# Performance work log

Hardware: AMD Instinct MI355X
Metric: run time of the kernel (lower is better)

Reference implementation:

```python
import jax, jax.numpy as jnp
import numpy as np

# Module hyperparameters (from init_kwargs)
B, C, T, H, W = 2, 128, 4, 64, 64
NHEADS = 32
SH, SW = 4, 4          # scales: patch size in H and W
GROUPS = C // 4        # GroupNorm groups = dim // 4
EPS = 1e-5


def _rel_index(t_, h_, w_):
    """(N,N) int32 index into the (2T-1)*(2h-1)*(2w-1) relative-position table."""
    tt = np.arange(t_); yy = np.arange(h_); xx = np.arange(w_)
    coords = np.stack(np.meshgrid(tt, yy, xx, indexing='ij'), -1).reshape(-1, 3)  # (N,3)
    rel = coords[:, None, :] - coords[None, :, :]                                 # (N,N,3)
    rel = rel + np.array([t_ - 1, h_ - 1, w_ - 1])
    idx = (rel[..., 0] * (2 * h_ - 1) + rel[..., 1]) * (2 * w_ - 1) + rel[..., 2]
    return idx.astype(np.int32)


def setup_inputs() -> dict:
    key = jax.random.key(0)
    ks = jax.random.split(key, 6)
    h, w = H // SH, W // SW
    table_sz = (2 * T - 1) * (2 * h - 1) * (2 * w - 1)
    inp = {
        "x": jax.random.normal(ks[0], (B, C, T, H, W), jnp.float32),
        "Wq": jax.random.normal(ks[1], (C, C), jnp.float32) / np.sqrt(C).astype(np.float32),
        "Wk": jax.random.normal(ks[2], (C, C), jnp.float32) / np.sqrt(C).astype(np.float32),
        "Wv": jax.random.normal(ks[3], (C, C), jnp.float32) / np.sqrt(C).astype(np.float32),
        "gq_gamma": jnp.ones((C,), jnp.float32), "gq_beta": jnp.zeros((C,), jnp.float32),
        "gk_gamma": jnp.ones((C,), jnp.float32), "gk_beta": jnp.zeros((C,), jnp.float32),
        "gv_gamma": jnp.ones((C,), jnp.float32), "gv_beta": jnp.zeros((C,), jnp.float32),
        "rel_table": jax.random.normal(ks[4], (NHEADS, table_sz), jnp.float32) * 0.02,
        "rel_index": jnp.asarray(_rel_index(T, h, w)),
    }
    return inp


def _group_norm(z, gamma, beta, groups, eps=EPS):
    b, c = z.shape[:2]
    zg = z.reshape(b, groups, c // groups, *z.shape[2:])
    mu = zg.mean(axis=(2, 3, 4, 5), keepdims=True)
    var = jnp.mean(jnp.square(zg - mu), axis=(2, 3, 4, 5), keepdims=True)
    zg = (zg - mu) * jax.lax.rsqrt(var + eps)
    zn = zg.reshape(z.shape)
    return zn * gamma[None, :, None, None, None] + beta[None, :, None, None, None]


def reference(x, Wq, Wk, Wv, gq_gamma, gq_beta, gk_gamma, gk_beta,
              gv_gamma, gv_beta, rel_table, rel_index):
    b, c, t, hh, ww = x.shape
    h, w = hh // SH, ww // SW
    n = t * h * w           # patch tokens
    p = SH * SW             # pixels per patch
    d = c // NHEADS         # head dim

    # 1x1x1 projections (pointwise conv == channel matmul) + GroupNorm
    q = _group_norm(jnp.einsum('bcthw,oc->bothw', x, Wq), gq_gamma, gq_beta, GROUPS)
    k = _group_norm(jnp.einsum('bcthw,oc->bothw', x, Wk), gk_gamma, gk_beta, GROUPS)
    v = _group_norm(jnp.einsum('bcthw,oc->bothw', x, Wv), gv_gamma, gv_beta, GROUPS)

    def to_patches(z):  # (b,c,t,H,W) -> (b,heads,d,N,P)
        z = z.reshape(b, NHEADS, d, t, h, SH, w, SW)
        z = z.transpose(0, 1, 2, 3, 4, 6, 5, 7)
        return z.reshape(b, NHEADS, d, n, p)

    qp = to_patches(q).mean(-1)     # pooled patch queries (b,g,d,N)
    kp = to_patches(k).mean(-1)     # pooled patch keys    (b,g,d,N)
    vp = to_patches(v)              # full-res values      (b,g,d,N,P)

    scale = 1.0 / jnp.sqrt(jnp.float32(d))
    logits = jnp.einsum('bgdn,bgdm->bgnm', qp, kp) * scale
    logits = logits + rel_table[:, rel_index][None]   # relative position bias (1,g,N,N)
    attn = jax.nn.softmax(logits, axis=-1)

    out = jnp.einsum('bgnm,bgdmp->bgdnp', attn, vp)   # (b,g,d,N,P)
    out = out.reshape(b, NHEADS, d, t, h, w, SH, SW).transpose(0, 1, 2, 3, 4, 6, 5, 7)
    out = out.reshape(b, c, t, hh, ww)                # (B,C,T,H,W) after outer permute
    return out
```

## Files before the change

kernel.cpp:

```cpp
#include <hip/hip_runtime.h>
#include <hip/hip_bf16.h>

#define B_ 2
#define C_ 128
#define G_ 32
#define N_ 1024
#define S_ 16384
#define TABLE_ 6727
#define EPS_ 1e-5f
#define LOG2E_ 1.44269504f
#define PSTB_ 64

typedef __hip_bfloat16 bf16;
typedef __attribute__((ext_vector_type(8))) short short8;
typedef __attribute__((ext_vector_type(4))) float f32x4;

#if __has_builtin(__builtin_amdgcn_exp2f)
#define EXP2(x) __builtin_amdgcn_exp2f(x)
#else
#define EXP2(x) __expf((x) * 0.69314718056f)
#endif

__device__ __forceinline__ float bf2f(bf16 v) { return __bfloat162float(v); }
__device__ __forceinline__ float bits2f(unsigned u) { return __uint_as_float(u); }
__device__ __forceinline__ int dflag(const void* gq) {
  return (((const unsigned*)gq)[0] != 0x3F803F80u) ? 1 : 0;
}
__device__ __forceinline__ float ldcv(const void* p, int i, int fl) {
  return fl ? ((const float*)p)[i] : bf2f(((const bf16*)p)[i]);
}

__global__ __launch_bounds__(256) void proj_kernel(
    const void* __restrict__ x, const void* __restrict__ Wq,
    const void* __restrict__ Wk, const void* __restrict__ Wv,
    const void* __restrict__ gq,
    bf16* __restrict__ qraw, bf16* __restrict__ kraw, bf16* __restrict__ vpt,
    float* __restrict__ statsAcc)
{
  __shared__ bf16 xs[128 * 128];
  __shared__ bf16 vs[8192];
  const int tid = threadIdx.x, lane = tid & 63, w = tid >> 6;
  const int s0 = blockIdx.x * 128;
  const int oh = blockIdx.y;
  const int b  = blockIdx.z;
  const int fl = dflag(gq);

  {
    const int s_lo = tid & 15, cb = tid >> 4;
    const size_t gc = (size_t)b * C_ * S_ + (size_t)(cb * 8) * S_ + s0 + s_lo;
#pragma unroll
    for (int i = 0; i < 8; ++i) {
      const int s = i * 16 + s_lo;
      union { short8 v; bf16 h[8]; } u;
      if (fl) {
#pragma unroll
        for (int j = 0; j < 8; ++j)
          u.h[j] = (bf16)((const float*)x)[gc + i * 16 + (size_t)j * S_];
      } else {
#pragma unroll
        for (int j = 0; j < 8; ++j)
          u.h[j] = ((const bf16*)x)[gc + i * 16 + (size_t)j * S_];
      }
      *(short8*)&xs[s * 128 + ((cb ^ (s & 7)) << 3)] = u.v;
    }
  }

  const int ow = oh * 4 + w;
  const int quad = lane >> 4;
  const int om = ow * 16 + (lane & 15);
  const void* const Ws[3] = {Wq, Wk, Wv};
  short8 afr[3][4];
#pragma unroll
  for (int tt = 0; tt < 3; ++tt)
#pragma unroll
    for (int kk = 0; kk < 4; ++kk) {
      const int off = om * 128 + kk * 32 + quad * 8;
      if (fl) {
        const float* wp = (const float*)Ws[tt] + off;
        const float4 a = *(const float4*)wp, bb = *(const float4*)(wp + 4);
        union { short8 s; bf16 h[8]; } u;
        u.h[0] = (bf16)a.x;  u.h[1] = (bf16)a.y;  u.h[2] = (bf16)a.z;  u.h[3] = (bf16)a.w;
        u.h[4] = (bf16)bb.x; u.h[5] = (bf16)bb.y; u.h[6] = (bf16)bb.z; u.h[7] = (bf16)bb.w;
        afr[tt][kk] = u.s;
      } else {
        afr[tt][kk] = *(const short8*)((const bf16*)Ws[tt] + off);
      }
    }
  __syncthreads();

  float ssum[3] = {0.f, 0.f, 0.f}, ssq[3] = {0.f, 0.f, 0.f};
  const int sl = lane & 15;
  for (int st = 0; st < 8; ++st) {
    f32x4 acc[3] = {{0,0,0,0},{0,0,0,0},{0,0,0,0}};
    const int srow = st * 16 + sl;
#pragma unroll
    for (int kk = 0; kk < 4; ++kk) {
      const short8 bv = *(const short8*)
          &xs[srow * 128 + ((((kk << 2) | quad) ^ (sl & 7)) << 3)];
      acc[0] = __builtin_amdgcn_mfma_f32_16x16x32_bf16(afr[0][kk], bv, acc[0], 0, 0, 0);
      acc[1] = __builtin_amdgcn_mfma_f32_16x16x32_bf16(afr[1][kk], bv, acc[1], 0, 0, 0);
      acc[2] = __builtin_amdgcn_mfma_f32_16x16x32_bf16(afr[2][kk], bv, acc[2], 0, 0, 0);
    }
    const int s = s0 + st * 16 + sl;
    const int pIdx = (st >> 2) * 4 + (sl & 3);
    const int xp = (st & 3) * 4 + (sl >> 2);
#pragma unroll
    for (int r = 0; r < 4; ++r) {
      const int o = ow * 16 + quad * 4 + r;
      const float vq = acc[0][r], vk = acc[1][r], vv = acc[2][r];
      ssum[0] += vq; ssq[0] += vq * vq;
      ssum[1] += vk; ssq[1] += vk * vk;
      ssum[2] += vv; ssq[2] += vv * vv;
      qraw[(size_t)(b * C_ + o) * S_ + s] = (bf16)vq;
      kraw[(size_t)(b * C_ + o) * S_ + s] = (bf16)vk;
      const int o_loc = w * 16 + quad * 4 + r;
      vs[(o_loc * 8 + pIdx) * 16 + xp] = (bf16)vv;
    }
  }
#pragma unroll
  for (int tt = 0; tt < 3; ++tt) {
#pragma unroll
    for (int off = 1; off < 16; off <<= 1) {
      ssum[tt] += __shfl_xor(ssum[tt], off);
      ssq[tt]  += __shfl_xor(ssq[tt], off);
    }
    if ((lane & 15) == 0) {
      const int grp = ow * 4 + quad;
      atomicAdd(&statsAcc[((tt * B_ + b) * G_ + grp) * 2 + 0], ssum[tt]);
      atomicAdd(&statsAcc[((tt * B_ + b) * G_ + grp) * 2 + 1], ssq[tt]);
    }
  }
  __syncthreads();

  const int rowp0 = (s0 >> 6) & 63;
  const int mIdx0 = (s0 >> 12) * 256 + (rowp0 >> 2) * 16;
  for (int cid = tid; cid < 1024; cid += 256) {
    const int half = cid & 1, run = cid >> 1;
    const int o_loc = run >> 3, pIdx = run & 7;
    const int o = oh * 64 + o_loc;
    const int gg = o >> 2, dd = o & 3;
    const int colv = dd * 16 + (rowp0 & 3) * 4 + pIdx;
    bf16* dst = vpt + ((size_t)(b * G_ + gg) * 64 + colv) * N_ + mIdx0 + half * 8;
    *(short8*)dst = *(const short8*)&vs[run * 16 + half * 8];
  }
}

__global__ __launch_bounds__(256) void pool_kernel(
    const bf16* __restrict__ qraw, const bf16* __restrict__ kraw,
    const void* __restrict__ gq, const void* __restrict__ bq,
    const void* __restrict__ gk, const void* __restrict__ bk,
    const float* __restrict__ statsAcc,
    bf16* __restrict__ qp2, bf16* __restrict__ kp2)
{
  const int fl = dflag(gq);
  const int idx = blockIdx.x * 256 + threadIdx.x;
  const int n = idx & 1023, d = (idx >> 10) & 3, g = (idx >> 12) & 31, b = idx >> 17;
  const int c = g * 4 + d;
  const int t = n >> 8, y = (n >> 4) & 15, xp = n & 15;
  const size_t base = (size_t)(b * C_ + c) * S_ + t * 4096 + y * 256 + xp * 4;
  float sq = 0.f, sk = 0.f;
#pragma unroll
  for (int sh = 0; sh < 4; ++sh) {
    const ushort4 uq = *(const ushort4*)(qraw + base + sh * 64);
    const ushort4 uk = *(const ushort4*)(kraw + base + sh * 64);
    sq += bits2f((unsigned)uq.x << 16) + bits2f((unsigned)uq.y << 16)
        + bits2f((unsigned)uq.z << 16) + bits2f((unsigned)uq.w << 16);
    sk += bits2f((unsigned)uk.x << 16) + bits2f((unsigned)uk.y << 16)
        + bits2f((unsigned)uk.z << 16) + bits2f((unsigned)uk.w << 16);
  }
  const float* saq = statsAcc + ((0 * B_ + b) * G_ + g) * 2;
  const float* sak = statsAcc + ((1 * B_ + b) * G_ + g) * 2;
  const float muq = saq[0] * (1.f / 65536.f);
  const float rq = rsqrtf(saq[1] * (1.f / 65536.f) - muq * muq + EPS_);
  const float muk = sak[0] * (1.f / 65536.f);
  const float rk = rsqrtf(sak[1] * (1.f / 65536.f) - muk * muk + EPS_);
  const float qn = (sq * 0.0625f - muq) * rq * ldcv(gq, c, fl) + ldcv(bq, c, fl);
  const float kn = (sk * 0.0625f - muk) * rk * ldcv(gk, c, fl) + ldcv(bk, c, fl);
  const float qs = qn * (0.5f * LOG2E_);
  const bf16 qh = (bf16)qs; const bf16 ql = (bf16)(qs - bf2f(qh));
  const bf16 kh = (bf16)kn; const bf16 kl = (bf16)(kn - bf2f(kh));
  const size_t qb = ((size_t)(b * G_ + g) * N_ + n) * 8;
  qp2[qb + d] = qh; qp2[qb + 4 + d] = ql;
  kp2[qb + d] = kh; kp2[qb + 4 + d] = kl;
}

__global__ __launch_bounds__(256, 4) void attn_kernel(
    const bf16* __restrict__ qp2, const bf16* __restrict__ kp2,
    const bf16* __restrict__ vpt, const void* __restrict__ rt,
    const void* __restrict__ gq, const void* __restrict__ gv,
    const void* __restrict__ bv, const float* __restrict__ statsAcc,
    void* __restrict__ outv)
{
  const int g = blockIdx.y, b = blockIdx.z;
  const int tid = threadIdx.x, lane = tid & 63, w = tid >> 6;
  const int nw = blockIdx.x * 64;
  const int fl = dflag(gq);
  __shared__ __align__(16) char smem[16384 + 5024 + 8192];
  bf16* Vlds = (bf16*)smem;
  bf16* bldm = (bf16*)(smem + 16384);
  bf16* pldw = (bf16*)(smem + 16384 + 5024) + w * 16 * PSTB_;

  const int tn = nw >> 8, yb = (nw >> 4) & 15;
  for (int i = tid; i < 2508; i += 256) {
    const int row = i / 33, d = i - row * 33;
    if (d < 31) {
      const int tm = row / 19, dyi = row - tm * 19;
      const int dt = tn - tm + 3;
      const int dy = yb + dyi;
      bldm[row * 33 + d] = (bf16)(ldcv(rt, g * TABLE_ + (dt * 31 + dy) * 31 + d, fl) * LOG2E_);
    }
  }

  const int col = lane & 15, quad = lane >> 4;
  const size_t bg = (size_t)(b * G_ + g);
  short8 af = {0, 0, 0, 0, 0, 0, 0, 0};
  if (quad < 2) af = *(const short8*)(qp2 + (bg * N_ + nw + w * 16 + col) * 8);

  const short* kpb = (const short*)kp2 + bg * N_ * 8;
  const short* vpb = (const short*)vpt + bg * 64 * N_;
  const short onebits = (short)0x3F80;
  const short8 ones8 = {onebits, onebits, onebits, onebits,
                        onebits, onebits, onebits, onebits};
  f32x4 acco[4] = {{0,0,0,0},{0,0,0,0},{0,0,0,0},{0,0,0,0}};
  f32x4 accs = {0.f, 0.f, 0.f, 0.f};

  const int skb = tid & 15, snr = tid >> 4;

  ushort4 kv[4], kvn[4];
#pragma unroll
  for (int t = 0; t < 4; ++t)
    kv[t] = *(const ushort4*)(kpb + ((0 * 4 + t) * 16 + col) * 8 + (quad & 1) * 4);

  for (int tile = 0; tile < 8; ++tile) {
    __syncthreads();
    short8 st[4];
#pragma unroll
    for (int i = 0; i < 4; ++i)
      st[i] = *(const short8*)(vpb + (size_t)(i * 16 + snr) * N_ + tile * 128 + skb * 8);
#pragma unroll
    for (int i = 0; i < 4; ++i) {
      const int n = i * 16 + snr;
      *(short8*)&Vlds[n * 128 + ((skb ^ (n & 7)) << 3)] = st[i];
    }
    __syncthreads();

    for (int cl = 0; cl < 2; ++cl) {
      const int ch = tile * 2 + cl;
      if (ch < 15) {
#pragma unroll
        for (int t = 0; t < 4; ++t)
          kvn[t] = *(const ushort4*)(kpb + (((ch + 1) * 4 + t) * 16 + col) * 8 + (quad & 1) * 4);
      }
#pragma unroll
      for (int mt4 = 0; mt4 < 4; ++mt4) {
        const int mt = ch * 4 + mt4;
        const int tm = mt >> 4, ym = mt & 15;
        const short8 bf8 = {(short)kv[mt4].x, (short)kv[mt4].y, (short)kv[mt4].z, (short)kv[mt4].w,
                            (short)kv[mt4].x, (short)kv[mt4].y, (short)kv[mt4].z, (short)kv[mt4].w};
        f32x4 acc = {0.f, 0.f, 0.f, 0.f};
        acc = __builtin_amdgcn_mfma_f32_16x16x32_bf16(af, bf8, acc, 0, 0, 0);
        const int bbase = (tm * 19 + (w + 15 - ym)) * 33 + 15 + quad * 4 - col;
#pragma unroll
        for (int r = 0; r < 4; ++r) {
          const float e = EXP2(acc[r] + bf2f(bldm[bbase + r]));
          const int row = quad * 4 + r;
          pldw[row * PSTB_ + (((mt4 * 2 + (col >> 3)) ^ (row & 7)) << 3) + (col & 7)] = (bf16)e;
        }
      }
#pragma unroll
      for (int ks = 0; ks < 2; ++ks) {
        const short8 a2 = *(const short8*)&pldw[col * PSTB_ + (((ks * 4 + quad) ^ (col & 7)) << 3)];
        accs = __builtin_amdgcn_mfma_f32_16x16x32_bf16(a2, ones8, accs, 0, 0, 0);
#pragma unroll
        for (int cc = 0; cc < 4; ++cc) {
          const int n = cc * 16 + col;
          const int kb = cl * 8 + ks * 4 + quad;
          const short8 b2 = *(const short8*)&Vlds[n * 128 + ((kb ^ (n & 7)) << 3)];
          acco[cc] = __builtin_amdgcn_mfma_f32_16x16x32_bf16(a2, b2, acco[cc], 0, 0, 0);
        }
      }
      if (ch < 15) {
#pragma unroll
        for (int t = 0; t < 4; ++t) kv[t] = kvn[t];
      }
    }
  }

  __syncthreads();
  const float* sav = statsAcc + ((2 * B_ + b) * G_ + g) * 2;
  const float mu = sav[0] * (1.f / 65536.f);
  const float rs = rsqrtf(sav[1] * (1.f / 65536.f) - mu * mu + EPS_);
  const int sh = col >> 2, sw = col & 3;
  const size_t obase = (size_t)(b * C_ + g * 4) * S_ + tn * 4096 + (yb + w) * 256;
  if (!fl) {
    bf16* ost = (bf16*)(smem + w * 2048);
#pragma unroll
    for (int cc = 0; cc < 4; ++cc) {
      const int c = g * 4 + cc;
      const float alpha = rs * ldcv(gv, c, fl);
      const float beta = ldcv(bv, c, fl) - mu * alpha;
#pragma unroll
      for (int r = 0; r < 4; ++r) {
        const int xp = quad * 4 + r;
        ost[cc * 256 + sh * 64 + xp * 4 + sw] = (bf16)(alpha * (acco[cc][r] / accs[r]) + beta);
      }
    }
#pragma unroll
    for (int i = 0; i < 2; ++i) {
      const int e = (i * 64 + lane) * 8;
      const int cc = e >> 8, rem = e & 255;
      *(short8*)((bf16*)outv + obase + (size_t)cc * S_ + rem) = *(const short8*)&ost[e];
    }
  } else {
    float* ostf = (float*)smem + w * 1024;
#pragma unroll
    for (int cc = 0; cc < 4; ++cc) {
      const int c = g * 4 + cc;
      const float alpha = rs * ldcv(gv, c, fl);
      const float beta = ldcv(bv, c, fl) - mu * alpha;
#pragma unroll
      for (int r = 0; r < 4; ++r) {
        const int xp = quad * 4 + r;
        ostf[cc * 256 + sh * 64 + xp * 4 + sw] = alpha * (acco[cc][r] / accs[r]) + beta;
      }
    }
#pragma unroll
    for (int i = 0; i < 4; ++i) {
      const int e = (i * 64 + lane) * 4;
      const int cc = e >> 8, rem = e & 255;
      *(float4*)((float*)outv + obase + (size_t)cc * S_ + rem) = *(const float4*)&ostf[e];
    }
  }
}

extern "C" void kernel_launch(void* const* d_in, const int* in_sizes, int n_in,
                              void* d_out, int out_size, void* d_ws, size_t ws_size,
                              hipStream_t stream) {
  (void)in_sizes; (void)n_in; (void)out_size; (void)ws_size;
  const void* x  = d_in[0];
  const void* Wq = d_in[1];
  const void* Wk = d_in[2];
  const void* Wv = d_in[3];
  const void* gq = d_in[4];
  const void* bq = d_in[5];
  const void* gk = d_in[6];
  const void* bk = d_in[7];
  const void* gv = d_in[8];
  const void* bv = d_in[9];
  const void* rel_table = d_in[10];

  bf16*  qraw = (bf16*)d_ws;
  bf16*  kraw = qraw + (size_t)B_ * C_ * S_;
  bf16*  vpt  = kraw + (size_t)B_ * C_ * S_;
  bf16*  qp2  = vpt  + (size_t)B_ * C_ * S_;
  bf16*  kp2  = qp2  + (size_t)B_ * G_ * N_ * 8;
  float* statsAcc = (float*)(kp2 + (size_t)B_ * G_ * N_ * 8);

  hipMemsetAsync(statsAcc, 0, 384 * sizeof(float), stream);
  proj_kernel<<<dim3(128, 2, B_), 256, 0, stream>>>(
      x, Wq, Wk, Wv, gq, qraw, kraw, vpt, statsAcc);
  pool_kernel<<<dim3(1024), 256, 0, stream>>>(
      qraw, kraw, gq, bq, gk, bk, statsAcc, qp2, kp2);
  attn_kernel<<<dim3(16, G_, B_), 256, 0, stream>>>(
      qp2, kp2, vpt, rel_table, gq, gv, bv, statsAcc, d_out);
}
```

Baseline: 168.8 us.

## Fuse patch pooling of q/k into projection kernel, drop full-res q/k writes

The projection kernel no longer writes full-resolution bf16 q and k to global memory. It sums each 4x4 patch in registers using lane shuffles and per-thread accumulators, then writes fp32 partial patch sums (two partials per patch) in an n-major, channel-minor layout. The pool kernel now only adds the two partials and applies the group-norm affine. This removes about 16 MB of write and read traffic, at the cost of extra shuffles and more register pressure from the fully unrolled loop.

Result: slower. 177.3 us (+5.0%).

```diff
diff --git a/kernel.cpp b/kernel.cpp
--- a/kernel.cpp
+++ b/kernel.cpp
@@ -34,8 +34,8 @@
     const void* __restrict__ x, const void* __restrict__ Wq,
     const void* __restrict__ Wk, const void* __restrict__ Wv,
     const void* __restrict__ gq,
-    bf16* __restrict__ qraw, bf16* __restrict__ kraw, bf16* __restrict__ vpt,
-    float* __restrict__ statsAcc)
+    float* __restrict__ qpart, float* __restrict__ kpart,
+    bf16* __restrict__ vpt, float* __restrict__ statsAcc)
 {
   __shared__ bf16 xs[128 * 128];
   __shared__ bf16 vs[8192];
@@ -89,7 +89,9 @@
   __syncthreads();
 
   float ssum[3] = {0.f, 0.f, 0.f}, ssq[3] = {0.f, 0.f, 0.f};
+  float psq[4][4] = {}, psk[4][4] = {};
   const int sl = lane & 15;
+#pragma unroll
   for (int st = 0; st < 8; ++st) {
     f32x4 acc[3] = {{0,0,0,0},{0,0,0,0},{0,0,0,0}};
     const int srow = st * 16 + sl;
@@ -101,22 +103,45 @@
       acc[1] = __builtin_amdgcn_mfma_f32_16x16x32_bf16(afr[1][kk], bv, acc[1], 0, 0, 0);
       acc[2] = __builtin_amdgcn_mfma_f32_16x16x32_bf16(afr[2][kk], bv, acc[2], 0, 0, 0);
     }
-    const int s = s0 + st * 16 + sl;
     const int pIdx = (st >> 2) * 4 + (sl & 3);
     const int xp = (st & 3) * 4 + (sl >> 2);
 #pragma unroll
     for (int r = 0; r < 4; ++r) {
-      const int o = ow * 16 + quad * 4 + r;
       const float vq = acc[0][r], vk = acc[1][r], vv = acc[2][r];
       ssum[0] += vq; ssq[0] += vq * vq;
       ssum[1] += vk; ssq[1] += vk * vk;
       ssum[2] += vv; ssq[2] += vv * vv;
-      qraw[(size_t)(b * C_ + o) * S_ + s] = (bf16)vq;
-      kraw[(size_t)(b * C_ + o) * S_ + s] = (bf16)vk;
+      float aq = vq + __shfl_xor(vq, 1); aq += __shfl_xor(aq, 2);
+      float ak = vk + __shfl_xor(vk, 1); ak += __shfl_xor(ak, 2);
+      psq[r][st & 3] += aq;
+      psk[r][st & 3] += ak;
       const int o_loc = w * 16 + quad * 4 + r;
       vs[(o_loc * 8 + pIdx) * 16 + xp] = (bf16)vv;
     }
   }
+
+  {
+    const int c = sl & 3, wxl = sl >> 2;
+    const int t = s0 >> 12;
+    const int yy0 = (s0 >> 6) & 63;
+    const int hy = yy0 >> 2, rp = (yy0 >> 1) & 1;
+    const int nbase = t * 256 + hy * 16;
+    const size_t pb = ((size_t)(b * 2 + rp) * N_ + nbase) * C_ + ow * 16 + quad * 4 + c;
+#pragma unroll
+    for (int j = 0; j < 4; ++j) {
+      float vq = psq[0][j];
+      if (c == 1) vq = psq[1][j];
+      if (c == 2) vq = psq[2][j];
+      if (c == 3) vq = psq[3][j];
+      float vk = psk[0][j];
+      if (c == 1) vk = psk[1][j];
+      if (c == 2) vk = psk[2][j];
+      if (c == 3) vk = psk[3][j];
+      qpart[pb + (size_t)(j * 4 + wxl) * C_] = vq;
+      kpart[pb + (size_t)(j * 4 + wxl) * C_] = vk;
+    }
+  }
+
 #pragma unroll
   for (int tt = 0; tt < 3; ++tt) {
 #pragma unroll
@@ -146,7 +171,7 @@
 }
 
 __global__ __launch_bounds__(256) void pool_kernel(
-    const bf16* __restrict__ qraw, const bf16* __restrict__ kraw,
+    const float* __restrict__ qpart, const float* __restrict__ kpart,
     const void* __restrict__ gq, const void* __restrict__ bq,
     const void* __restrict__ gk, const void* __restrict__ bk,
     const float* __restrict__ statsAcc,
@@ -154,20 +179,12 @@
 {
   const int fl = dflag(gq);
   const int idx = blockIdx.x * 256 + threadIdx.x;
-  const int n = idx & 1023, d = (idx >> 10) & 3, g = (idx >> 12) & 31, b = idx >> 17;
-  const int c = g * 4 + d;
-  const int t = n >> 8, y = (n >> 4) & 15, xp = n & 15;
-  const size_t base = (size_t)(b * C_ + c) * S_ + t * 4096 + y * 256 + xp * 4;
-  float sq = 0.f, sk = 0.f;
-#pragma unroll
-  for (int sh = 0; sh < 4; ++sh) {
-    const ushort4 uq = *(const ushort4*)(qraw + base + sh * 64);
-    const ushort4 uk = *(const ushort4*)(kraw + base + sh * 64);
-    sq += bits2f((unsigned)uq.x << 16) + bits2f((unsigned)uq.y << 16)
-        + bits2f((unsigned)uq.z << 16) + bits2f((unsigned)uq.w << 16);
-    sk += bits2f((unsigned)uk.x << 16) + bits2f((unsigned)uk.y << 16)
-        + bits2f((unsigned)uk.z << 16) + bits2f((unsigned)uk.w << 16);
-  }
+  const int c = idx & 127, n = (idx >> 7) & 1023, b = idx >> 17;
+  const int g = c >> 2, d = c & 3;
+  const size_t p0 = ((size_t)(b * 2 + 0) * N_ + n) * C_ + c;
+  const size_t p1 = ((size_t)(b * 2 + 1) * N_ + n) * C_ + c;
+  const float sq = qpart[p0] + qpart[p1];
+  const float sk = kpart[p0] + kpart[p1];
   const float* saq = statsAcc + ((0 * B_ + b) * G_ + g) * 2;
   const float* sak = statsAcc + ((1 * B_ + b) * G_ + g) * 2;
   const float muq = saq[0] * (1.f / 65536.f);
@@ -349,18 +366,18 @@
   const void* bv = d_in[9];
   const void* rel_table = d_in[10];
 
-  bf16*  qraw = (bf16*)d_ws;
-  bf16*  kraw = qraw + (size_t)B_ * C_ * S_;
-  bf16*  vpt  = kraw + (size_t)B_ * C_ * S_;
-  bf16*  qp2  = vpt  + (size_t)B_ * C_ * S_;
+  bf16*  vpt  = (bf16*)d_ws;
+  bf16*  qp2  = vpt  + (size_t)B_ * G_ * 64 * N_;
   bf16*  kp2  = qp2  + (size_t)B_ * G_ * N_ * 8;
-  float* statsAcc = (float*)(kp2 + (size_t)B_ * G_ * N_ * 8);
+  float* qpart = (float*)(kp2 + (size_t)B_ * G_ * N_ * 8);
+  float* kpart = qpart + (size_t)B_ * 2 * N_ * C_;
+  float* statsAcc = kpart + (size_t)B_ * 2 * N_ * C_;
 
   hipMemsetAsync(statsAcc, 0, 384 * sizeof(float), stream);
   proj_kernel<<<dim3(128, 2, B_), 256, 0, stream>>>(
-      x, Wq, Wk, Wv, gq, qraw, kraw, vpt, statsAcc);
+      x, Wq, Wk, Wv, gq, qpart, kpart, vpt, statsAcc);
   pool_kernel<<<dim3(1024), 256, 0, stream>>>(
-      qraw, kraw, gq, bq, gk, bk, statsAcc, qp2, kp2);
+      qpart, kpart, gq, bq, gk, bk, statsAcc, qp2, kp2);
   attn_kernel<<<dim3(16, G_, B_), 256, 0, stream>>>(
       qp2, kp2, vpt, rel_table, gq, gv, bv, statsAcc, d_out);
 }
```
